# Optimization experiments

Measured on AMD Instinct MI355X. Metric: run time of the kernel, lower is better.

## Reference

```python
import jax, jax.numpy as jnp
import numpy as np

HID = 4096; NH = 32; NKV = 8; HD = 128; EPS = 1e-6; BASE = 10000.0

def _rmsnorm(x, w):
    # RMSNorm over last (head_dim) axis
    return x * jax.lax.rsqrt(jnp.mean(x * x, axis=-1, keepdims=True) + EPS) * w

def _rope(x, positions):
    # neox-style rotary on (b, s, h, HD): rotate halves
    half = HD // 2
    inv_freq = 1.0 / (BASE ** (jnp.arange(0, HD, 2, dtype=jnp.float32) / HD))  # (half,)
    ang = positions.astype(jnp.float32)[:, None] * inv_freq                    # (s, half)
    cos = jnp.cos(ang)[None, :, None, :]
    sin = jnp.sin(ang)[None, :, None, :]
    x1, x2 = x[..., :half], x[..., half:]
    return jnp.concatenate([x1 * cos - x2 * sin, x2 * cos + x1 * sin], axis=-1)

def setup_inputs() -> dict:
    key = jax.random.key(0)
    k0, k1, k2 = jax.random.split(key, 3)
    b, s = 4, 1024
    return {
        "h_shard": jax.random.normal(k0, (b, s, HID), jnp.float32),
        "positions": jnp.arange(s, dtype=jnp.int32),
        "w_qkv": jax.random.normal(k1, (NH * HD + 2 * NKV * HD, HID), jnp.float32) * 0.02,
        "w_o": jax.random.normal(k2, (HID, NH * HD), jnp.float32) * 0.02,
        "q_norm_w": jnp.ones((HD,), jnp.float32),
        "k_norm_w": jnp.ones((HD,), jnp.float32),
    }

def reference(h_shard, positions, w_qkv, w_o, q_norm_w, k_norm_w):
    b, s, _ = h_shard.shape
    q_sz, kv_sz = NH * HD, NKV * HD
    # fused QKV projection (world_size=1 -> ag_mm is a plain matmul x @ W.T)
    qkv = h_shard @ w_qkv.T                                   # (b, s, q_sz + 2*kv_sz)
    q = qkv[..., :q_sz].reshape(b, s, NH, HD)
    k = qkv[..., q_sz:q_sz + kv_sz].reshape(b, s, NKV, HD)
    v = qkv[..., q_sz + kv_sz:].reshape(b, s, NKV, HD)
    # per-head RMSNorm then RoPE on q/k (Qwen3 ordering)
    q = _rope(_rmsnorm(q, q_norm_w), positions)
    k = _rope(_rmsnorm(k, k_norm_w), positions)
    # GQA SDPA without materializing repeated KV: group query heads per kv head
    g = NH // NKV
    qg = q.reshape(b, s, NKV, g, HD)
    scores = jnp.einsum('bskgd,btkd->bkgst', qg, k) / jnp.sqrt(jnp.float32(HD))
    causal = jnp.tril(jnp.ones((s, s), dtype=bool))
    scores = jnp.where(causal, scores, -jnp.inf)
    probs = jax.nn.softmax(scores, axis=-1)
    attn = jnp.einsum('bkgst,btkd->bskgd', probs, v).reshape(b, s, q_sz)
    # output projection (mm_rs -> plain matmul for world_size=1)
    return attn @ w_o.T
```

## Files before the change

### kernel.cpp

```cpp
#include <hip/hip_runtime.h>

typedef __bf16 bf16;
typedef __bf16 bf16x4 __attribute__((ext_vector_type(4)));
typedef __bf16 bf16x8 __attribute__((ext_vector_type(8)));
typedef float f32x4 __attribute__((ext_vector_type(4)));

#define HID 4096
#define QKV_N 6144
#define NTOK 4096

#define SB()  __builtin_amdgcn_sched_barrier(0)
#define BAR() __builtin_amdgcn_s_barrier()

__device__ __forceinline__ void gload_lds16(const bf16* g, bf16* l) {
  __builtin_amdgcn_global_load_lds(
      (__attribute__((address_space(1))) void*)(g),
      (__attribute__((address_space(3))) void*)(l), 16, 0, 0);
}

__global__ void cvt_kernel(const float4* __restrict__ s, bf16x4* __restrict__ d) {
  int i = blockIdx.x * blockDim.x + threadIdx.x;
  float4 v = s[i];
  bf16x4 o;
  o[0] = (bf16)v.x; o[1] = (bf16)v.y; o[2] = (bf16)v.z; o[3] = (bf16)v.w;
  d[i] = o;
}

template <typename OutT>
__global__ __launch_bounds__(512, 2) void gemm_bt256(
    const bf16* __restrict__ A, const bf16* __restrict__ Bm,
    OutT* __restrict__ C, int M, int N, int K)
{
  __shared__ __align__(16) bf16 As[2][256 * 64];
  __shared__ __align__(16) bf16 Bs[2][256 * 64];

  const int tid = threadIdx.x;
  const int w = tid >> 6, l = tid & 63;
  const int quad = l >> 4, lane16 = l & 15;
  const int sw = lane16 & 7;
  const int lrow = l >> 3;
  const int lk = (l & 7) ^ lrow;

  const int nwg = gridDim.x * gridDim.y;
  int bid = blockIdx.y * gridDim.x + blockIdx.x;
  bid = (bid & 7) * (nwg >> 3) + (bid >> 3);
  const int row0 = (bid / gridDim.x) * 256;
  const int col0 = (bid % gridDim.x) * 256;

  const int wm = (w >> 2) * 128;
  const int wn = (w & 3) * 64;

  f32x4 acc[2][2][4][2];
#pragma unroll
  for (int mq = 0; mq < 2; ++mq)
#pragma unroll
    for (int nq = 0; nq < 2; ++nq)
#pragma unroll
      for (int im = 0; im < 4; ++im)
#pragma unroll
        for (int in_ = 0; in_ < 2; ++in_) acc[mq][nq][im][in_] = (f32x4){0.f, 0.f, 0.f, 0.f};

  bf16x8 aF0[4][2], aF1[4][2];
  bf16x8 bF0[2][2], bF1[2][2];

  auto stA = [&](int buf, int half, int kt) {
    const bf16* g = A + (size_t)(row0 + half * 128 + w * 8 + lrow) * K + kt * 64 + lk * 8;
    bf16* s = &As[buf][(half * 128 + w * 8) * 64 + l * 8];
    gload_lds16(g, s);
    gload_lds16(g + (size_t)64 * K, s + 64 * 64);
  };
  auto stB = [&](int buf, int half, int kt) {
    const bf16* g = Bm + (size_t)(col0 + half * 128 + w * 8 + lrow) * K + kt * 64 + lk * 8;
    bf16* s = &Bs[buf][(half * 128 + w * 8) * 64 + l * 8];
    gload_lds16(g, s);
    gload_lds16(g + (size_t)64 * K, s + 64 * 64);
  };

  auto loadA = [&](const bf16* Ap, bf16x8 (&dst)[4][2], int mq) {
#pragma unroll
    for (int im = 0; im < 4; ++im)
#pragma unroll
      for (int kk = 0; kk < 2; ++kk)
        dst[im][kk] = *(const bf16x8*)&Ap[(wm + mq * 64 + im * 16 + lane16) * 64 +
                                          (((kk * 4 + quad) ^ sw) * 8)];
  };
  auto loadB = [&](const bf16* Bp, bf16x8 (&dst)[2][2], int nq) {
#pragma unroll
    for (int in_ = 0; in_ < 2; ++in_)
#pragma unroll
      for (int kk = 0; kk < 2; ++kk)
        dst[in_][kk] = *(const bf16x8*)&Bp[(wn + nq * 32 + in_ * 16 + lane16) * 64 +
                                           (((kk * 4 + quad) ^ sw) * 8)];
  };
  auto mma = [&](bf16x8 (&a)[4][2], bf16x8 (&b)[2][2], f32x4 (&ac)[4][2]) {
#pragma unroll
    for (int im = 0; im < 4; ++im)
#pragma unroll
      for (int in_ = 0; in_ < 2; ++in_) {
        ac[im][in_] = __builtin_amdgcn_mfma_f32_16x16x32_bf16(a[im][0], b[in_][0], ac[im][in_], 0, 0, 0);
        ac[im][in_] = __builtin_amdgcn_mfma_f32_16x16x32_bf16(a[im][1], b[in_][1], ac[im][in_], 0, 0, 0);
      }
  };

  const int nt = K >> 6;

  stB(0, 0, 0); stB(0, 1, 0); stA(0, 0, 0); stA(0, 1, 0);
  if (nt > 1) {
    stB(1, 0, 1); stB(1, 1, 1); stA(1, 0, 1); stA(1, 1, 1);
    asm volatile("s_waitcnt vmcnt(8)" ::: "memory");
  } else {
    asm volatile("s_waitcnt vmcnt(0)" ::: "memory");
  }
  BAR();
  SB();
  loadA(As[0], aF0, 0);

  for (int t = 0; t < nt; ++t) {
    const int p = t & 1;
    const bf16* Ap = As[p];
    const bf16* Bp = Bs[p];

    loadB(Bp, bF0, 0);
    loadB(Bp, bF1, 1);
    SB(); BAR(); SB();
    __builtin_amdgcn_s_setprio(1);
    mma(aF0, bF0, acc[0][0]);
    __builtin_amdgcn_s_setprio(0);
    SB(); BAR(); SB();

    loadA(Ap, aF1, 1);
    SB(); BAR(); SB();
    __builtin_amdgcn_s_setprio(1);
    mma(aF0, bF1, acc[0][1]);
    __builtin_amdgcn_s_setprio(0);
    SB(); BAR(); SB();

    if (t + 2 < nt) { stB(p, 0, t + 2); stB(p, 1, t + 2); }
    SB(); BAR(); SB();
    __builtin_amdgcn_s_setprio(1);
    mma(aF1, bF1, acc[1][1]);
    __builtin_amdgcn_s_setprio(0);
    SB();
    if (t + 2 < nt) asm volatile("s_waitcnt vmcnt(4)" ::: "memory");
    else            asm volatile("s_waitcnt vmcnt(0)" ::: "memory");
    BAR(); SB();

    if (t + 1 < nt) loadA(As[p ^ 1], aF0, 0);
    if (t + 2 < nt) { stA(p, 0, t + 2); stA(p, 1, t + 2); }
    SB(); BAR(); SB();
    __builtin_amdgcn_s_setprio(1);
    mma(aF1, bF0, acc[1][0]);
    __builtin_amdgcn_s_setprio(0);
    SB(); BAR(); SB();
  }

#pragma unroll
  for (int mq = 0; mq < 2; ++mq)
#pragma unroll
    for (int im = 0; im < 4; ++im)
#pragma unroll
      for (int r = 0; r < 4; ++r) {
        int row = row0 + wm + mq * 64 + im * 16 + quad * 4 + r;
        OutT* cp = C + (size_t)row * N + col0 + wn;
#pragma unroll
        for (int nq = 0; nq < 2; ++nq)
#pragma unroll
          for (int in_ = 0; in_ < 2; ++in_)
            cp[nq * 32 + in_ * 16 + lane16] = (OutT)acc[mq][nq][im][in_][r];
      }
}

__global__ __launch_bounds__(256) void norm_rope_kernel(
    bf16* __restrict__ qkv, const int* __restrict__ pos,
    const float* __restrict__ qw, const float* __restrict__ kw)
{
  int g = blockIdx.x * 4 + (threadIdx.x >> 6);
  int tok = g / 40;
  int slot = g % 40;
  int d = threadIdx.x & 63;
  bf16* base;
  const float* w;
  if (slot < 32) { base = qkv + (size_t)tok * QKV_N + slot * 128; w = qw; }
  else           { base = qkv + (size_t)tok * QKV_N + HID + (slot - 32) * 128; w = kw; }
  float x1 = (float)base[d], x2 = (float)base[d + 64];
  float ss = x1 * x1 + x2 * x2;
#pragma unroll
  for (int m = 1; m < 64; m <<= 1) ss += __shfl_xor(ss, m, 64);
  float rn = rsqrtf(ss * (1.0f / 128.0f) + 1e-6f);
  x1 = x1 * rn * w[d];
  x2 = x2 * rn * w[d + 64];
  int p = pos[tok & 1023];
  float invf = exp2f(-0.20762050593045952f * (float)d);
  float ang = (float)p * invf;
  float sn, c;
  sincosf(ang, &sn, &c);
  base[d]      = (bf16)(x1 * c - x2 * sn);
  base[d + 64] = (bf16)(x2 * c + x1 * sn);
}

__global__ __launch_bounds__(256) void flash_kernel(
    const bf16* __restrict__ qkv, bf16* __restrict__ attn)
{
  __shared__ bf16 Ks[2][64 * 128];
  __shared__ bf16 Vt[2][128 * 64];
  __shared__ bf16 Ps[4][16 * 72];

  const int bh = blockIdx.y;
  const int qt = ((bh >> 4) & 1) ? (15 - blockIdx.x) : blockIdx.x;
  const int batch = bh >> 5;
  const int qh = bh & 31;
  const int kvh = qh >> 2;
  const int tid = threadIdx.x;
  const int w = tid >> 6, l = tid & 63;
  const int quad = l >> 4, lane16 = l & 15;
  const int sw = lane16 & 7;
  const size_t tok0 = (size_t)batch * 1024;
  const int q0 = qt * 64;

  bf16x8 qf[4];
  {
    const bf16* qrow = qkv + (tok0 + q0 + w * 16 + lane16) * QKV_N + qh * 128 + quad * 8;
#pragma unroll
    for (int kk = 0; kk < 4; ++kk) qf[kk] = *(const bf16x8*)(qrow + kk * 32);
  }

  f32x4 O[8];
#pragma unroll
  for (int id = 0; id < 8; ++id) O[id] = (f32x4){0.f, 0.f, 0.f, 0.f};
  float m_run[4], l_run[4];
#pragma unroll
  for (int r = 0; r < 4; ++r) { m_run[r] = -1e30f; l_run[r] = 0.f; }

  const float scale = 0.08838834764831845f;
  bf16x8 vreg[4];

  auto stage_K = [&](int j, int buf) {
#pragma unroll
    for (int r = 0; r < 4; ++r) {
      int i = r * 4 + w;
      int rloc = i * 4 + (l >> 4);
      int o = (l & 15) ^ (rloc & 7);
      const bf16* g = qkv + (tok0 + j * 64 + rloc) * QKV_N + HID + kvh * 128 + o * 8;
      gload_lds16(g, &Ks[buf][i * 512 + l * 8]);
    }
  };
  auto load_V = [&](int j) {
#pragma unroll
    for (int c = 0; c < 4; ++c) {
      int d0 = (c * 4 + w) * 8;
      vreg[c] = *(const bf16x8*)(qkv + (tok0 + j * 64 + l) * QKV_N + HID + 1024 + kvh * 128 + d0);
    }
  };
  auto write_V = [&](int buf) {
#pragma unroll
    for (int c = 0; c < 4; ++c) {
      int d0 = (c * 4 + w) * 8;
#pragma unroll
      for (int e = 0; e < 8; ++e) {
        int d = d0 + e;
        Vt[buf][d * 64 + (((l >> 3) ^ (d & 7)) * 8) + (l & 7)] = vreg[c][e];
      }
    }
  };

  stage_K(0, 0);
  load_V(0);
  write_V(0);
  __syncthreads();

  for (int j = 0; j <= qt; ++j) {
    const int p = j & 1;
    if (j < qt) { stage_K(j + 1, p ^ 1); load_V(j + 1); }

    f32x4 s[4];
#pragma unroll
    for (int in_ = 0; in_ < 4; ++in_) s[in_] = (f32x4){0.f, 0.f, 0.f, 0.f};
#pragma unroll
    for (int kk = 0; kk < 4; ++kk) {
#pragma unroll
      for (int in_ = 0; in_ < 4; ++in_) {
        bf16x8 b = *(const bf16x8*)&Ks[p][(in_ * 16 + lane16) * 128 + (((kk * 4 + quad) ^ sw) * 8)];
        s[in_] = __builtin_amdgcn_mfma_f32_16x16x32_bf16(qf[kk], b, s[in_], 0, 0, 0);
      }
    }

    if (j < qt) write_V(p ^ 1);

    const bool edge = (j == qt);
#pragma unroll
    for (int r = 0; r < 4; ++r) {
      float rm = -1e30f;
#pragma unroll
      for (int in_ = 0; in_ < 4; ++in_) {
        float v = s[in_][r] * scale;
        if (edge) {
          int t_abs = j * 64 + in_ * 16 + lane16;
          int q_abs = q0 + w * 16 + quad * 4 + r;
          v = (t_abs <= q_abs) ? v : -1e30f;
        }
        s[in_][r] = v;
        rm = fmaxf(rm, v);
      }
#pragma unroll
      for (int m = 1; m < 16; m <<= 1) rm = fmaxf(rm, __shfl_xor(rm, m, 64));
      float mn = fmaxf(m_run[r], rm);
      float alpha = __expf(m_run[r] - mn);
      m_run[r] = mn;
      float rs = 0.f;
#pragma unroll
      for (int in_ = 0; in_ < 4; ++in_) {
        float pv = __expf(s[in_][r] - mn);
        s[in_][r] = pv;
        rs += pv;
      }
#pragma unroll
      for (int m = 1; m < 16; m <<= 1) rs += __shfl_xor(rs, m, 64);
      l_run[r] = l_run[r] * alpha + rs;
#pragma unroll
      for (int id = 0; id < 8; ++id) O[id][r] *= alpha;
#pragma unroll
      for (int in_ = 0; in_ < 4; ++in_)
        Ps[w][(quad * 4 + r) * 72 + in_ * 16 + lane16] = (bf16)s[in_][r];
    }

#pragma unroll
    for (int kt = 0; kt < 2; ++kt) {
      bf16x8 a = *(const bf16x8*)&Ps[w][lane16 * 72 + kt * 32 + quad * 8];
#pragma unroll
      for (int id = 0; id < 8; ++id) {
        bf16x8 b = *(const bf16x8*)&Vt[p][(id * 16 + lane16) * 64 + (((kt * 4 + quad) ^ sw) * 8)];
        O[id] = __builtin_amdgcn_mfma_f32_16x16x32_bf16(a, b, O[id], 0, 0, 0);
      }
    }
    __syncthreads();
  }

#pragma unroll
  for (int r = 0; r < 4; ++r) {
    float inv = 1.0f / l_run[r];
    int row = q0 + w * 16 + quad * 4 + r;
    bf16* orow = attn + (tok0 + row) * (size_t)HID + qh * 128;
#pragma unroll
    for (int id = 0; id < 8; ++id) orow[id * 16 + lane16] = (bf16)(O[id][r] * inv);
  }
}

extern "C" void kernel_launch(void* const* d_in, const int* in_sizes, int n_in,
                              void* d_out, int out_size, void* d_ws, size_t ws_size,
                              hipStream_t stream) {
  const float* h    = (const float*)d_in[0];
  const int*   pos  = (const int*)d_in[1];
  const float* wqkv = (const float*)d_in[2];
  const float* wo   = (const float*)d_in[3];
  const float* qw   = (const float*)d_in[4];
  const float* kw   = (const float*)d_in[5];
  float* out = (float*)d_out;

  bf16* hb    = (bf16*)d_ws;
  bf16* wqkvb = hb + 16777216;
  bf16* wob   = wqkvb + 25165824;
  bf16* qkvb  = wob + 16777216;
  bf16* attnb = qkvb + 25165824;

  cvt_kernel<<<16384, 256, 0, stream>>>((const float4*)h, (bf16x4*)hb);
  cvt_kernel<<<24576, 256, 0, stream>>>((const float4*)wqkv, (bf16x4*)wqkvb);
  cvt_kernel<<<16384, 256, 0, stream>>>((const float4*)wo, (bf16x4*)wob);

  gemm_bt256<bf16><<<dim3(24, 16), 512, 0, stream>>>(hb, wqkvb, qkvb, NTOK, QKV_N, HID);

  norm_rope_kernel<<<NTOK * 40 / 4, 256, 0, stream>>>(qkvb, pos, qw, kw);

  flash_kernel<<<dim3(16, 128), 256, 0, stream>>>(qkvb, attnb);

  gemm_bt256<float><<<dim3(16, 16), 512, 0, stream>>>(attnb, wob, out, NTOK, HID, HID);
}
```

Measured before the change: 804.8 us.

## Interleave GEMM global-to-LDS loads per quadrant and remap warp tiles to split halves

Reworks the 256x256 GEMM main loop. Each of the four MFMA phases now issues one half-tile global-to-LDS prefetch, with explicit vmcnt/lgkmcnt waits replacing sched_barriers and bulk prefetches. Warp sub-tiles are remapped so each warp's two M and N fragments sit in separate 128-row halves of the tile, which matches the half-granular load order. The aim is to spread memory traffic evenly across compute phases. It also drops the nt>1 guard and re-loads the last tile redundantly near the end, and the hand-placed waitcnt values could be wrong.

Result: no change. 803.2 us (-0.2%).

```diff
diff --git a/kernel.cpp b/kernel.cpp
--- a/kernel.cpp
+++ b/kernel.cpp
@@ -9,7 +9,6 @@
 #define QKV_N 6144
 #define NTOK 4096
 
-#define SB()  __builtin_amdgcn_sched_barrier(0)
 #define BAR() __builtin_amdgcn_s_barrier()
 
 __device__ __forceinline__ void gload_lds16(const bf16* g, bf16* l) {
@@ -47,8 +46,8 @@
   const int row0 = (bid / gridDim.x) * 256;
   const int col0 = (bid % gridDim.x) * 256;
 
-  const int wm = (w >> 2) * 128;
-  const int wn = (w & 3) * 64;
+  const int wm = (w >> 2) * 64;
+  const int wn = (w & 3) * 32;
 
   f32x4 acc[2][2][4][2];
 #pragma unroll
@@ -76,20 +75,20 @@
     gload_lds16(g + (size_t)64 * K, s + 64 * 64);
   };
 
-  auto loadA = [&](const bf16* Ap, bf16x8 (&dst)[4][2], int mq) {
+  auto loadAF = [&](const bf16* Ap, bf16x8 (&dst)[4][2], int mq) {
 #pragma unroll
     for (int im = 0; im < 4; ++im)
 #pragma unroll
       for (int kk = 0; kk < 2; ++kk)
-        dst[im][kk] = *(const bf16x8*)&Ap[(wm + mq * 64 + im * 16 + lane16) * 64 +
+        dst[im][kk] = *(const bf16x8*)&Ap[(mq * 128 + wm + im * 16 + lane16) * 64 +
                                           (((kk * 4 + quad) ^ sw) * 8)];
   };
-  auto loadB = [&](const bf16* Bp, bf16x8 (&dst)[2][2], int nq) {
+  auto loadBF = [&](const bf16* Bp, bf16x8 (&dst)[2][2], int nq) {
 #pragma unroll
     for (int in_ = 0; in_ < 2; ++in_)
 #pragma unroll
       for (int kk = 0; kk < 2; ++kk)
-        dst[in_][kk] = *(const bf16x8*)&Bp[(wn + nq * 32 + in_ * 16 + lane16) * 64 +
+        dst[in_][kk] = *(const bf16x8*)&Bp[(nq * 128 + wn + in_ * 16 + lane16) * 64 +
                                            (((kk * 4 + quad) ^ sw) * 8)];
   };
   auto mma = [&](bf16x8 (&a)[4][2], bf16x8 (&b)[2][2], f32x4 (&ac)[4][2]) {
@@ -104,54 +103,58 @@
 
   const int nt = K >> 6;
 
-  stB(0, 0, 0); stB(0, 1, 0); stA(0, 0, 0); stA(0, 1, 0);
-  if (nt > 1) {
-    stB(1, 0, 1); stB(1, 1, 1); stA(1, 0, 1); stA(1, 1, 1);
-    asm volatile("s_waitcnt vmcnt(8)" ::: "memory");
-  } else {
-    asm volatile("s_waitcnt vmcnt(0)" ::: "memory");
-  }
+  stA(0, 0, 0); stB(0, 0, 0); stB(0, 1, 0); stA(0, 1, 0);
+  stA(1, 0, 1); stB(1, 0, 1); stB(1, 1, 1); stA(1, 1, 1);
+  asm volatile("s_waitcnt vmcnt(12)" ::: "memory");
   BAR();
-  SB();
-  loadA(As[0], aF0, 0);
+  loadAF(As[0], aF0, 0);
+  asm volatile("s_waitcnt lgkmcnt(0)" ::: "memory");
+  BAR();
 
   for (int t = 0; t < nt; ++t) {
     const int p = t & 1;
     const bf16* Ap = As[p];
     const bf16* Bp = Bs[p];
-
-    loadB(Bp, bF0, 0);
-    loadB(Bp, bF1, 1);
-    SB(); BAR(); SB();
+    const int kt = (t + 2 < nt) ? (t + 2) : (nt - 1);
+
+    loadBF(Bp, bF0, 0);
+    stA(p, 0, kt);
+    BAR();
+    asm volatile("s_waitcnt lgkmcnt(0)" ::: "memory");
     __builtin_amdgcn_s_setprio(1);
     mma(aF0, bF0, acc[0][0]);
     __builtin_amdgcn_s_setprio(0);
-    SB(); BAR(); SB();
-
-    loadA(Ap, aF1, 1);
-    SB(); BAR(); SB();
+    asm volatile("s_waitcnt vmcnt(4)" ::: "memory");
+    BAR();
+
+    loadBF(Bp, bF1, 1);
+    stB(p, 0, kt);
+    BAR();
+    asm volatile("s_waitcnt lgkmcnt(0)" ::: "memory");
     __builtin_amdgcn_s_setprio(1);
     mma(aF0, bF1, acc[0][1]);
     __builtin_amdgcn_s_setprio(0);
-    SB(); BAR(); SB();
-
-    if (t + 2 < nt) { stB(p, 0, t + 2); stB(p, 1, t + 2); }
-    SB(); BAR(); SB();
+    asm volatile("s_waitcnt vmcnt(4)" ::: "memory");
+    BAR();
+
+    loadAF(Ap, aF1, 1);
+    stB(p, 1, kt);
+    BAR();
+    asm volatile("s_waitcnt lgkmcnt(0)" ::: "memory");
     __builtin_amdgcn_s_setprio(1);
     mma(aF1, bF1, acc[1][1]);
     __builtin_amdgcn_s_setprio(0);
-    SB();
-    if (t + 2 < nt) asm volatile("s_waitcnt vmcnt(4)" ::: "memory");
-    else            asm volatile("s_waitcnt vmcnt(0)" ::: "memory");
-    BAR(); SB();
-
-    if (t + 1 < nt) loadA(As[p ^ 1], aF0, 0);
-    if (t + 2 < nt) { stA(p, 0, t + 2); stA(p, 1, t + 2); }
-    SB(); BAR(); SB();
+    asm volatile("s_waitcnt vmcnt(4)" ::: "memory");
+    BAR();
+
+    if (t + 1 < nt) loadAF(As[p ^ 1], aF0, 0);
+    stA(p, 1, kt);
+    BAR();
     __builtin_amdgcn_s_setprio(1);
     mma(aF1, bF0, acc[1][0]);
     __builtin_amdgcn_s_setprio(0);
-    SB(); BAR(); SB();
+    asm volatile("s_waitcnt vmcnt(4) lgkmcnt(0)" ::: "memory");
+    BAR();
   }
 
 #pragma unroll
@@ -160,13 +163,13 @@
     for (int im = 0; im < 4; ++im)
 #pragma unroll
       for (int r = 0; r < 4; ++r) {
-        int row = row0 + wm + mq * 64 + im * 16 + quad * 4 + r;
+        int row = row0 + mq * 128 + wm + im * 16 + quad * 4 + r;
         OutT* cp = C + (size_t)row * N + col0 + wn;
 #pragma unroll
         for (int nq = 0; nq < 2; ++nq)
 #pragma unroll
           for (int in_ = 0; in_ < 2; ++in_)
-            cp[nq * 32 + in_ * 16 + lane16] = (OutT)acc[mq][nq][im][in_][r];
+            cp[nq * 128 + in_ * 16 + lane16] = (OutT)acc[mq][nq][im][in_][r];
       }
 }
 
```
